# Kernel tuning notes

Hardware: AMD Instinct MI355X
Metric: run time of the kernel (lower is better)

## Reference

```python
import jax, jax.numpy as jnp
import numpy as np

# ---- constants (from init_kwargs / Config) ----
C = 10            # number of classes
P = 128           # fixed prototype capacity per class (masked)
GAMMA = 0.1
B_CONST = 10.0    # b
TAO = 1.0
BETA = 1.0
LAMBDA = 0.1
THRESHOLD = 40.0
EPS = 1e-6        # nn.PairwiseDistance eps (added to the difference)


def setup_inputs() -> dict:
    key = jax.random.key(0)
    k1, k2 = jax.random.split(key)
    features = jax.random.normal(k1, (8192, 512), dtype=jnp.float32)
    labels = jax.random.randint(k2, (8192,), 0, C, dtype=jnp.int32)
    return {"features": features, "labels": labels}


def _assign_prototypes(features, labels):
    """Sequential prototype assignment (faithful to assign_prototype).
    Fixed-capacity store: protos [C,P,D], counts [C,P], nproto [C]."""
    D = features.shape[1]
    protos = jnp.zeros((C, P, D), features.dtype)
    counts = jnp.zeros((C, P), jnp.int32)
    nproto = jnp.zeros((C,), jnp.int32)

    def step(carry, xs):
        protos, counts, nproto = carry
        f, l = xs
        row = protos[l]                       # [P, D]
        cnt = counts[l]                       # [P]
        n = nproto[l]
        valid = jnp.arange(P) < n
        d2 = jnp.sum((f[None, :] - row + EPS) ** 2, axis=-1)
        d2m = jnp.where(valid, d2, jnp.inf)
        idx = jnp.argmin(d2m)
        dmin = jnp.sqrt(d2m[idx])
        do_update = (n > 0) & (dmin < THRESHOLD)
        # running-mean update of closest prototype
        c = cnt[idx].astype(f.dtype)
        new_val = (row[idx] * c + f) / (c + 1.0)
        app_idx = jnp.minimum(n, P - 1)       # append slot (clamped; never hit with these settings)
        tgt_idx = jnp.where(do_update, idx, app_idx)
        tgt_val = jnp.where(do_update, new_val, f)
        tgt_cnt = jnp.where(do_update, cnt[idx] + 1, 1)
        row = row.at[tgt_idx].set(tgt_val)
        cnt = cnt.at[tgt_idx].set(tgt_cnt)
        n = jnp.where(do_update, n, jnp.minimum(n + 1, P))
        protos = protos.at[l].set(row)
        counts = counts.at[l].set(cnt)
        nproto = nproto.at[l].set(n)
        return (protos, counts, nproto), None

    (protos, counts, nproto), _ = jax.lax.scan(step, (protos, counts, nproto), (features, labels))
    return protos, nproto


def _forward(features, labels):
    # assign_prototype uses tensor(features).detach() -> stop_gradient
    protos, nproto = _assign_prototypes(jax.lax.stop_gradient(features), labels)
    B, D = features.shape
    flat = protos.reshape(C * P, D)
    valid = (jnp.arange(P)[None, :] < nproto[:, None]).reshape(C * P)

    # squared PairwiseDistance with eps added to the difference:
    # sum((f - p + eps)^2) = |f|^2 + |p|^2 - 2 f.p + 2*eps*(sum f - sum p) + D*eps^2
    f2 = jnp.sum(features ** 2, axis=-1)          # [B]
    p2 = jnp.sum(flat ** 2, axis=-1)              # [C*P]
    sf = jnp.sum(features, axis=-1)
    sp = jnp.sum(flat, axis=-1)
    d2 = (f2[:, None] + p2[None, :] - 2.0 * (features @ flat.T)
          + 2.0 * EPS * (sf[:, None] - sp[None, :]) + D * EPS * EPS)
    d2 = jnp.maximum(d2, 0.0)                     # [B, C*P]

    # dce loss: probability = 1e-6 + sum_label exp(-g d^2) / sum_all exp(-g d^2)
    expv = jnp.where(valid[None, :], jnp.exp(-GAMMA * d2), 0.0)
    per_class = expv.reshape(B, C, P).sum(-1)     # [B, C]
    one = per_class.sum(-1)                       # [B]
    num = jnp.take_along_axis(per_class, labels[:, None].astype(jnp.int32), axis=1)[:, 0]
    prob = 1e-6 + jnp.where(one > 0.0, num / one, one)
    dce_loss = jnp.sum(-jnp.log(prob))

    # pairwise loss: per sample, per existing class, min distance
    d2c = jnp.where(valid[None, :], d2, jnp.inf).reshape(B, C, P).min(-1)
    dmin = jnp.sqrt(d2c)                          # [B, C]
    sign = jnp.where(labels[:, None] == jnp.arange(C)[None, :], 1.0, -1.0)
    z = B_CONST - (TAO - dmin) * sign
    g = jnp.where(z > 10.0, z, jax.nn.softplus(BETA * z) / BETA)
    exists = nproto > 0                           # only classes present in all_prototypes
    pw_loss = jnp.sum(jnp.where(exists[None, :], g, 0.0))

    return dce_loss + LAMBDA * pw_loss


def reference(features, labels):
    return _forward(features, labels)
```

## Files before the change

kernel.cpp:

```cpp
#include <hip/hip_runtime.h>
#include <math.h>

#define NC 10
#define NP 128
#define ND 512
#define GAMMA  0.1f
#define BCONST 10.0f
#define TAO    1.0f
#define LAMBDA 0.1f
#define THR2   1600.0f
#define FEPS   1e-6f
#define NLDS   12
#define CH     16
#define MAXCH  512
#define IMAX   0x7FFFFFFF

__device__ __forceinline__ float allred64(float v) {
#pragma unroll
  for (int m = 1; m < 64; m <<= 1) v += __shfl_xor(v, m, 64);
  return v;
}

__global__ __launch_bounds__(256)
void ord_kernel(const int* __restrict__ labels, int B,
                int* __restrict__ order, int* __restrict__ cls_base,
                int* __restrict__ cls_cnt, int* __restrict__ fail_pos,
                int* __restrict__ nproto_g, float* __restrict__ out)
{
  __shared__ int lab[8192];
  __shared__ int wtot[4][NC];
  const int t = threadIdx.x, lane = t & 63, w = t >> 6;

  if (t < NC) { fail_pos[t] = IMAX; nproto_g[t] = 0; }
  if (t == 0) out[0] = 0.f;

  const int4* lp = (const int4*)labels;
  for (int i = t; i < (B >> 2); i += 256) {
    int4 v = lp[i];
    lab[i*4+0] = v.x; lab[i*4+1] = v.y; lab[i*4+2] = v.z; lab[i*4+3] = v.w;
  }
  for (int i = (B & ~3) + t; i < B; i += 256) lab[i] = labels[i];
  __syncthreads();

  const int segsz = (B + 255) >> 8;
  const int s0 = t * segsz, s1 = min(s0 + segsz, B);

  int loc[NC];
#pragma unroll
  for (int c = 0; c < NC; ++c) loc[c] = 0;
  for (int i = s0; i < s1; ++i) {
    int l = lab[i];
#pragma unroll
    for (int c = 0; c < NC; ++c) loc[c] += (l == c) ? 1 : 0;
  }

  int pre[NC];
#pragma unroll
  for (int c = 0; c < NC; ++c) pre[c] = loc[c];
#pragma unroll
  for (int m = 1; m < 64; m <<= 1) {
#pragma unroll
    for (int c = 0; c < NC; ++c) {
      int u = __shfl_up(pre[c], m, 64);
      if (lane >= m) pre[c] += u;
    }
  }
  if (lane == 63) {
#pragma unroll
    for (int c = 0; c < NC; ++c) wtot[w][c] = pre[c];
  }
  __syncthreads();

  int pos[NC];
  {
    int cb = 0;
#pragma unroll
    for (int c = 0; c < NC; ++c) {
      int tot = wtot[0][c] + wtot[1][c] + wtot[2][c] + wtot[3][c];
      int before = 0;
#pragma unroll
      for (int ww = 0; ww < 4; ++ww) before += (ww < w) ? wtot[ww][c] : 0;
      pos[c] = cb + before + (pre[c] - loc[c]);
      if (t == 0) { cls_base[c] = cb; cls_cnt[c] = tot; }
      cb += tot;
    }
  }

  for (int i = s0; i < s1; ++i) {
    int l = lab[i];
#pragma unroll
    for (int c = 0; c < NC; ++c)
      if (l == c) order[pos[c]++] = i;
  }
}

__global__ __launch_bounds__(64)
void chunksum_kernel(const float* __restrict__ feats, const int* __restrict__ order,
                     const int* __restrict__ cls_base, const int* __restrict__ cls_cnt,
                     float* __restrict__ chunksum)
{
  const int c = blockIdx.x / MAXCH, g = blockIdx.x % MAXCH;
  const int cnt = cls_cnt[c];
  const int nch = (cnt + CH - 1) / CH;
  if (g >= nch) return;
  const int base = cls_base[c], lane = threadIdx.x;
  const int k0 = g * CH, k1 = min(k0 + CH, cnt);
  int myidx = (lane < CH && k0 + lane < cnt) ? order[base + k0 + lane] : 0;

  float S[8] = {0, 0, 0, 0, 0, 0, 0, 0};
  int k = k0;
  for (; k + 4 <= k1; k += 4) {
    float4 A[4], Bv[4];
#pragma unroll
    for (int j = 0; j < 4; ++j) {
      int idx = __shfl(myidx, k + j - k0, 64);
      const float4* fp = (const float4*)(feats + (size_t)idx * ND + lane * 8);
      A[j] = fp[0]; Bv[j] = fp[1];
    }
#pragma unroll
    for (int j = 0; j < 4; ++j) {
      S[0]+=A[j].x; S[1]+=A[j].y; S[2]+=A[j].z; S[3]+=A[j].w;
      S[4]+=Bv[j].x; S[5]+=Bv[j].y; S[6]+=Bv[j].z; S[7]+=Bv[j].w;
    }
  }
  for (; k < k1; ++k) {
    int idx = __shfl(myidx, k - k0, 64);
    const float4* fp = (const float4*)(feats + (size_t)idx * ND + lane * 8);
    float4 a = fp[0], b = fp[1];
    S[0]+=a.x; S[1]+=a.y; S[2]+=a.z; S[3]+=a.w;
    S[4]+=b.x; S[5]+=b.y; S[6]+=b.z; S[7]+=b.w;
  }
  float4* cp = (float4*)(chunksum + ((size_t)c * MAXCH + g) * ND + lane * 8);
  cp[0] = make_float4(S[0], S[1], S[2], S[3]);
  cp[1] = make_float4(S[4], S[5], S[6], S[7]);
}

__global__ __launch_bounds__(64)
void verify_kernel(const float* __restrict__ feats, const int* __restrict__ order,
                   const int* __restrict__ cls_base, const int* __restrict__ cls_cnt,
                   const float* __restrict__ chunksum, int* __restrict__ fail_pos,
                   float* __restrict__ gproto, float* __restrict__ p2s,
                   float* __restrict__ sps, int* __restrict__ nproto_g)
{
  const int c = blockIdx.x / MAXCH, g = blockIdx.x % MAXCH;
  const int cnt = cls_cnt[c];
  const int nch = (cnt + CH - 1) / CH;
  if (g >= nch) return;
  const int base = cls_base[c], lane = threadIdx.x;
  const int k0 = g * CH, k1 = min(k0 + CH, cnt);
  int myidx = (lane < CH && k0 + lane < cnt) ? order[base + k0 + lane] : 0;

  float P[8] = {0, 0, 0, 0, 0, 0, 0, 0};
  {
    const float* cbase = chunksum + (size_t)c * MAXCH * ND + lane * 8;
    int j = 0;
    for (; j + 4 <= g; j += 4) {
      float4 A[4], Bv[4];
#pragma unroll
      for (int q = 0; q < 4; ++q) {
        const float4* pp = (const float4*)(cbase + (size_t)(j + q) * ND);
        A[q] = pp[0]; Bv[q] = pp[1];
      }
#pragma unroll
      for (int q = 0; q < 4; ++q) {
        P[0]+=A[q].x; P[1]+=A[q].y; P[2]+=A[q].z; P[3]+=A[q].w;
        P[4]+=Bv[q].x; P[5]+=Bv[q].y; P[6]+=Bv[q].z; P[7]+=Bv[q].w;
      }
    }
    for (; j < g; ++j) {
      const float4* pp = (const float4*)(cbase + (size_t)j * ND);
      float4 a = pp[0], b = pp[1];
      P[0]+=a.x; P[1]+=a.y; P[2]+=a.z; P[3]+=a.w;
      P[4]+=b.x; P[5]+=b.y; P[6]+=b.z; P[7]+=b.w;
    }
  }

  int k = k0;
  for (; k + 4 <= k1; k += 4) {
    float4 A[4], Bv[4];
#pragma unroll
    for (int j = 0; j < 4; ++j) {
      int idx = __shfl(myidx, k + j - k0, 64);
      const float4* fp = (const float4*)(feats + (size_t)idx * ND + lane * 8);
      A[j] = fp[0]; Bv[j] = fp[1];
    }
    float part[4];
#pragma unroll
    for (int j = 0; j < 4; ++j) {
      int kk = k + j;
      float f[8] = {A[j].x, A[j].y, A[j].z, A[j].w, Bv[j].x, Bv[j].y, Bv[j].z, Bv[j].w};
      if (kk > 0) {
        float inv = 1.f / (float)kk;
        float p = 0.f;
#pragma unroll
        for (int e = 0; e < 8; ++e) { float d = f[e] - P[e] * inv + FEPS; p += d * d; }
        part[j] = p;
      } else part[j] = 0.f;
#pragma unroll
      for (int e = 0; e < 8; ++e) P[e] += f[e];
    }
#pragma unroll
    for (int m = 1; m < 64; m <<= 1) {
#pragma unroll
      for (int j = 0; j < 4; ++j) part[j] += __shfl_xor(part[j], m, 64);
    }
    if (lane == 0) {
#pragma unroll
      for (int j = 0; j < 4; ++j) {
        int kk = k + j;
        if (kk > 0 && !(part[j] < THR2)) atomicMin(&fail_pos[c], kk);
      }
    }
  }
  for (; k < k1; ++k) {
    int idx = __shfl(myidx, k - k0, 64);
    const float4* fp = (const float4*)(feats + (size_t)idx * ND + lane * 8);
    float4 fa = fp[0], fb = fp[1];
    float f[8] = {fa.x, fa.y, fa.z, fa.w, fb.x, fb.y, fb.z, fb.w};
    if (k > 0) {
      float inv = 1.f / (float)k;
      float p = 0.f;
#pragma unroll
      for (int e = 0; e < 8; ++e) { float d = f[e] - P[e] * inv + FEPS; p += d * d; }
      float d2 = allred64(p);
      if (!(d2 < THR2) && lane == 0) atomicMin(&fail_pos[c], k);
    }
#pragma unroll
    for (int e = 0; e < 8; ++e) P[e] += f[e];
  }

  if (g == nch - 1) {
    float inv = 1.f / (float)cnt;
    float p[8];
#pragma unroll
    for (int e = 0; e < 8; ++e) p[e] = P[e] * inv;
    float4* gp = (float4*)(gproto + (size_t)c * NP * ND + lane * 8);
    gp[0] = make_float4(p[0], p[1], p[2], p[3]);
    gp[1] = make_float4(p[4], p[5], p[6], p[7]);
    float P2p = 0.f, SPp = 0.f;
#pragma unroll
    for (int e = 0; e < 8; ++e) { P2p += p[e]*p[e]; SPp += p[e]; }
    float P2 = allred64(P2p), SP = allred64(SPp);
    if (lane == 0) { p2s[c*NP] = P2; sps[c*NP] = SP; nproto_g[c] = 1; }
  }
}

__global__ __launch_bounds__(64)
void fallback_kernel(const float* __restrict__ feats, const int* __restrict__ order,
                     const int* __restrict__ cls_base, const int* __restrict__ cls_cnt,
                     const int* __restrict__ fail_pos,
                     float* __restrict__ gproto, float* __restrict__ p2s,
                     float* __restrict__ sps, int* __restrict__ nproto_g)
{
  const int c = blockIdx.x;
  if (fail_pos[c] == IMAX) return;

  __shared__ float ls_proto[NLDS][ND];
  __shared__ int   ls_cnt[NP];
  const int lane = threadIdx.x;
  const int base = cls_base[c], cnt = cls_cnt[c];

  float p0[8];
  int cnt0 = 0, n = 0;
  float fA[8], fB[8], fC[8];

  auto LOADF = [&](float (&buf)[8], int m) {
    int idx = order[base + m];
    const float4* fp = (const float4*)(feats + (size_t)idx * ND + lane * 8);
    float4 a = fp[0], b = fp[1];
    buf[0]=a.x; buf[1]=a.y; buf[2]=a.z; buf[3]=a.w;
    buf[4]=b.x; buf[5]=b.y; buf[6]=b.z; buf[7]=b.w;
  };

  auto STEP = [&](float (&f)[8]) {
    float best = 3.4e38f;
    int bidx = 0;
    if (n > 0) {
      float part = 0.f;
#pragma unroll
      for (int e = 0; e < 8; ++e) { float d = f[e] - p0[e] + FEPS; part += d * d; }
      best = allred64(part);
      for (int j = 1; j < n; ++j) {
        float pj[8];
        if (j <= NLDS) {
          const float4* pp = (const float4*)(&ls_proto[j-1][lane*8]);
          float4 a = pp[0], b = pp[1];
          pj[0]=a.x; pj[1]=a.y; pj[2]=a.z; pj[3]=a.w;
          pj[4]=b.x; pj[5]=b.y; pj[6]=b.z; pj[7]=b.w;
        } else {
          const float4* pp = (const float4*)(gproto + ((size_t)c*NP + j)*ND + lane*8);
          float4 a = pp[0], b = pp[1];
          pj[0]=a.x; pj[1]=a.y; pj[2]=a.z; pj[3]=a.w;
          pj[4]=b.x; pj[5]=b.y; pj[6]=b.z; pj[7]=b.w;
        }
        float part2 = 0.f;
#pragma unroll
        for (int e = 0; e < 8; ++e) { float d = f[e] - pj[e] + FEPS; part2 += d * d; }
        float tot = allred64(part2);
        if (tot < best) { best = tot; bidx = j; }
      }
    }
    if (n > 0 && best < THR2) {
      if (bidx == 0) {
        float cc = (float)cnt0, inv = 1.f / (cc + 1.f);
#pragma unroll
        for (int e = 0; e < 8; ++e) p0[e] = (p0[e]*cc + f[e]) * inv;
        cnt0++;
      } else {
        int ci = ls_cnt[bidx];
        float cc = (float)ci, inv = 1.f / (cc + 1.f);
        if (bidx <= NLDS) {
          float* row = &ls_proto[bidx-1][lane*8];
#pragma unroll
          for (int e = 0; e < 8; ++e) row[e] = (row[e]*cc + f[e]) * inv;
        } else {
          float* row = gproto + ((size_t)c*NP + bidx)*ND + lane*8;
#pragma unroll
          for (int e = 0; e < 8; ++e) row[e] = (row[e]*cc + f[e]) * inv;
        }
        if (lane == 0) ls_cnt[bidx] = ci + 1;
      }
    } else {
      int app = min(n, NP - 1);
      if (app == 0) {
#pragma unroll
        for (int e = 0; e < 8; ++e) p0[e] = f[e];
        cnt0 = 1;
      } else if (app <= NLDS) {
        float* row = &ls_proto[app-1][lane*8];
#pragma unroll
        for (int e = 0; e < 8; ++e) row[e] = f[e];
        if (lane == 0) ls_cnt[app] = 1;
      } else {
        float* row = gproto + ((size_t)c*NP + app)*ND + lane*8;
#pragma unroll
        for (int e = 0; e < 8; ++e) row[e] = f[e];
        if (lane == 0) ls_cnt[app] = 1;
      }
      n = min(n + 1, NP);
    }
  };

  if (cnt > 0) LOADF(fA, 0);
  if (cnt > 1) LOADF(fB, 1);
  if (cnt > 2) LOADF(fC, 2);
  int m = 0;
  while (m < cnt) {
    STEP(fA); ++m; if (m + 2 < cnt) LOADF(fA, m + 2);
    if (m >= cnt) break;
    STEP(fB); ++m; if (m + 2 < cnt) LOADF(fB, m + 2);
    if (m >= cnt) break;
    STEP(fC); ++m; if (m + 2 < cnt) LOADF(fC, m + 2);
  }

  for (int j = 0; j < n; ++j) {
    float pj[8];
    if (j == 0) {
#pragma unroll
      for (int e = 0; e < 8; ++e) pj[e] = p0[e];
    } else if (j <= NLDS) {
      const float4* pp = (const float4*)(&ls_proto[j-1][lane*8]);
      float4 a = pp[0], b = pp[1];
      pj[0]=a.x; pj[1]=a.y; pj[2]=a.z; pj[3]=a.w;
      pj[4]=b.x; pj[5]=b.y; pj[6]=b.z; pj[7]=b.w;
    } else {
      const float4* pp = (const float4*)(gproto + ((size_t)c*NP + j)*ND + lane*8);
      float4 a = pp[0], b = pp[1];
      pj[0]=a.x; pj[1]=a.y; pj[2]=a.z; pj[3]=a.w;
      pj[4]=b.x; pj[5]=b.y; pj[6]=b.z; pj[7]=b.w;
    }
    float4* gp = (float4*)(gproto + ((size_t)c*NP + j)*ND + lane*8);
    gp[0] = make_float4(pj[0], pj[1], pj[2], pj[3]);
    gp[1] = make_float4(pj[4], pj[5], pj[6], pj[7]);
    float P2p = 0.f, SPp = 0.f;
#pragma unroll
    for (int e = 0; e < 8; ++e) { P2p += pj[e]*pj[e]; SPp += pj[e]; }
    float P2 = allred64(P2p), SP = allred64(SPp);
    if (lane == 0) { p2s[c*NP + j] = P2; sps[c*NP + j] = SP; }
  }
  if (lane == 0) nproto_g[c] = n;
}

__global__ __launch_bounds__(256)
void loss_kernel(const float* __restrict__ feats, const int* __restrict__ labels, int B,
                 const float* __restrict__ gproto, const float* __restrict__ p2s,
                 const float* __restrict__ sps, const int* __restrict__ nproto_g,
                 float* __restrict__ out)
{
  __shared__ float bsum[4];
  const int lane = threadIdx.x & 63;
  const int wid  = threadIdx.x >> 6;
  const int gw   = blockIdx.x * 4 + wid;
  const int nw   = gridDim.x * 4;

  int np[NC];
  bool fast = true;
#pragma unroll
  for (int cc = 0; cc < NC; ++cc) { np[cc] = nproto_g[cc]; fast &= (np[cc] == 1); }

  float acc = 0.f;

  if (fast) {
    float p2v[NC], spv[NC];
#pragma unroll
    for (int cc = 0; cc < NC; ++cc) { p2v[cc] = p2s[cc*NP]; spv[cc] = sps[cc*NP]; }

    for (int b = gw; b < B; b += nw) {
      const float4* fp = (const float4*)(feats + (size_t)b * ND + lane * 8);
      float4 a4 = fp[0], b4 = fp[1];
      float f[8] = {a4.x, a4.y, a4.z, a4.w, b4.x, b4.y, b4.z, b4.w};
      int lab = labels[b];

      float v[12];
#pragma unroll
      for (int cc = 0; cc < NC; ++cc) {
        const float4* pp = (const float4*)(gproto + (size_t)cc * NP * ND + lane * 8);
        float4 pa = pp[0], pb = pp[1];
        v[cc] = f[0]*pa.x + f[1]*pa.y + f[2]*pa.z + f[3]*pa.w
              + f[4]*pb.x + f[5]*pb.y + f[6]*pb.z + f[7]*pb.w;
      }
      float f2p = 0.f, sfp = 0.f;
#pragma unroll
      for (int e = 0; e < 8; ++e) { f2p += f[e]*f[e]; sfp += f[e]; }
      v[10] = f2p; v[11] = sfp;

#pragma unroll
      for (int m = 1; m < 64; m <<= 1) {
#pragma unroll
        for (int q = 0; q < 12; ++q) v[q] += __shfl_xor(v[q], m, 64);
      }
      float f2 = v[10], sf = v[11];

      float one = 0.f, num = 0.f, pw = 0.f;
#pragma unroll
      for (int cc = 0; cc < NC; ++cc) {
        float d2 = f2 + p2v[cc] - 2.f*v[cc]
                 + 2.f*FEPS*(sf - spv[cc]) + (float)ND*FEPS*FEPS;
        d2 = fmaxf(d2, 0.f);
        float e = expf(-GAMMA * d2);
        one += e;
        if (cc == lab) num = e;
        float dmin = sqrtf(d2);
        float sign = (cc == lab) ? 1.f : -1.f;
        float z = BCONST - (TAO - dmin) * sign;
        float gg = (z > 10.f) ? z : log1pf(expf(z));
        pw += gg;
      }
      float prob = 1e-6f + ((one > 0.f) ? num / one : one);
      acc += -logf(prob) + LAMBDA * pw;
    }
  } else {
    for (int b = gw; b < B; b += nw) {
      const float4* fp = (const float4*)(feats + (size_t)b * ND + lane * 8);
      float4 a4 = fp[0], b4 = fp[1];
      float f[8] = {a4.x, a4.y, a4.z, a4.w, b4.x, b4.y, b4.z, b4.w};
      float f2p = 0.f, sfp = 0.f;
#pragma unroll
      for (int e = 0; e < 8; ++e) { f2p += f[e]*f[e]; sfp += f[e]; }
      float f2 = allred64(f2p);
      float sf = allred64(sfp);
      int lab = labels[b];

      float one = 0.f, num = 0.f, pw = 0.f;
      for (int cc = 0; cc < NC; ++cc) {
        int nn = np[cc];
        if (nn <= 0) continue;
        float sume = 0.f, bestd2 = 3.4e38f;
        for (int j = 0; j < nn; ++j) {
          const float4* pp = (const float4*)(gproto + ((size_t)cc*NP + j)*ND + lane*8);
          float4 pa = pp[0], pb = pp[1];
          float dp = f[0]*pa.x + f[1]*pa.y + f[2]*pa.z + f[3]*pa.w
                   + f[4]*pb.x + f[5]*pb.y + f[6]*pb.z + f[7]*pb.w;
          float dot = allred64(dp);
          float d2 = f2 + p2s[cc*NP + j] - 2.f*dot
                   + 2.f*FEPS*(sf - sps[cc*NP + j]) + (float)ND*FEPS*FEPS;
          d2 = fmaxf(d2, 0.f);
          sume  += expf(-GAMMA * d2);
          bestd2 = fminf(bestd2, d2);
        }
        one += sume;
        if (cc == lab) num = sume;
        float dmin = sqrtf(bestd2);
        float sign = (cc == lab) ? 1.f : -1.f;
        float z = BCONST - (TAO - dmin) * sign;
        float g = (z > 10.f) ? z : log1pf(expf(z));
        pw += g;
      }
      float prob = 1e-6f + ((one > 0.f) ? num / one : one);
      acc += -logf(prob) + LAMBDA * pw;
    }
  }

  if (lane == 0) bsum[wid] = acc;
  __syncthreads();
  if (threadIdx.x == 0) atomicAdd(out, bsum[0] + bsum[1] + bsum[2] + bsum[3]);
}

extern "C" void kernel_launch(void* const* d_in, const int* in_sizes, int n_in,
                              void* d_out, int out_size, void* d_ws, size_t ws_size,
                              hipStream_t stream) {
  const float* feats  = (const float*)d_in[0];
  const int*   labels = (const int*)d_in[1];
  int B = in_sizes[0] / ND;

  float* gproto   = (float*)d_ws;
  float* p2s      = gproto + (size_t)NC * NP * ND;
  float* sps      = p2s + NC * NP;
  float* chunksum = sps + NC * NP;
  int*   nproto_g = (int*)(chunksum + (size_t)NC * MAXCH * ND);
  int*   order    = nproto_g + NC;
  int*   cls_base = order + B;
  int*   cls_cnt  = cls_base + NC;
  int*   fail_pos = cls_cnt + NC;

  hipLaunchKernelGGL(ord_kernel, dim3(1), dim3(256), 0, stream,
                     labels, B, order, cls_base, cls_cnt, fail_pos,
                     nproto_g, (float*)d_out);
  hipLaunchKernelGGL(chunksum_kernel, dim3(NC * MAXCH), dim3(64), 0, stream,
                     feats, order, cls_base, cls_cnt, chunksum);
  hipLaunchKernelGGL(verify_kernel, dim3(NC * MAXCH), dim3(64), 0, stream,
                     feats, order, cls_base, cls_cnt, chunksum, fail_pos,
                     gproto, p2s, sps, nproto_g);
  hipLaunchKernelGGL(fallback_kernel, dim3(NC), dim3(64), 0, stream,
                     feats, order, cls_base, cls_cnt, fail_pos,
                     gproto, p2s, sps, nproto_g);
  hipLaunchKernelGGL(loss_kernel, dim3(2048), dim3(256), 0, stream,
                     feats, labels, B, gproto, p2s, sps, nproto_g, (float*)d_out);
}
```

Measured before the change: 88.82 us.

## Merge ordering, chunk-sum and fallback kernels into two compact-grid kernels

Drops the separate single-block label-ordering kernel and the fallback kernel. Each block of the chunk-sum and verify kernels now recomputes the per-class compaction into shared memory. Work is mapped onto a dense grid of 131 blocks with 4 waves each, instead of 5120 single-wave blocks where most exit early. The fallback now runs in the last-finishing wave of each failing class, found with a done counter, which cuts kernel launches and wasted block scheduling. The cost is that every block redundantly scans all the labels, and the fallback path leans on atomics and fences between waves of different blocks.

Measured after the change: 106.7 us. 20.1% more time.

```diff
diff --git a/kernel.cpp b/kernel.cpp
--- a/kernel.cpp
+++ b/kernel.cpp
@@ -12,100 +12,88 @@
 #define FEPS   1e-6f
 #define NLDS   12
 #define CH     16
-#define MAXCH  512
+#define WPB    4
+#define NBLK   131
 #define IMAX   0x7FFFFFFF
 
-__device__ __forceinline__ float allred64(float v) {
+__device__ __forceinline__ float allredf(float v) {
 #pragma unroll
   for (int m = 1; m < 64; m <<= 1) v += __shfl_xor(v, m, 64);
   return v;
 }
 
+#define COMPACT_BODY                                                          \
+  const int t = threadIdx.x, lane = t & 63, w = t >> 6;                       \
+  {                                                                           \
+    const int segsz = (B + 255) >> 8;                                         \
+    const int i0 = t * segsz, i1 = min(i0 + segsz, B);                        \
+    int loc[NC];                                                              \
+    _Pragma("unroll") for (int c = 0; c < NC; ++c) loc[c] = 0;                \
+    for (int i = i0; i < i1; ++i) {                                           \
+      int l = labels[i];                                                      \
+      _Pragma("unroll") for (int c = 0; c < NC; ++c) loc[c] += (l == c);      \
+    }                                                                         \
+    int pre[NC];                                                              \
+    _Pragma("unroll") for (int c = 0; c < NC; ++c) pre[c] = loc[c];           \
+    _Pragma("unroll") for (int m = 1; m < 64; m <<= 1) {                      \
+      _Pragma("unroll") for (int c = 0; c < NC; ++c) {                        \
+        int u = __shfl_up(pre[c], m, 64);                                     \
+        if (lane >= m) pre[c] += u;                                           \
+      }                                                                       \
+    }                                                                         \
+    if (lane == 63) {                                                         \
+      _Pragma("unroll") for (int c = 0; c < NC; ++c) wtot[w][c] = pre[c];     \
+    }                                                                         \
+    __syncthreads();                                                          \
+    int pos[NC];                                                              \
+    {                                                                         \
+      int cb = 0, crun = 0;                                                   \
+      _Pragma("unroll") for (int c = 0; c < NC; ++c) {                        \
+        int tot = wtot[0][c] + wtot[1][c] + wtot[2][c] + wtot[3][c];          \
+        int before = 0;                                                       \
+        _Pragma("unroll") for (int ww = 0; ww < 4; ++ww)                      \
+          before += (ww < w) ? wtot[ww][c] : 0;                               \
+        pos[c] = cb + before + (pre[c] - loc[c]);                             \
+        if (t == 0) { cb_s[c] = cb; cc_s[c] = tot; chb_s[c] = crun; }         \
+        cb += tot;                                                            \
+        crun += (tot + CH - 1) / CH;                                          \
+      }                                                                       \
+      if (t == 0) nchtot_s = crun;                                            \
+    }                                                                         \
+    for (int i = i0; i < i1; ++i) {                                           \
+      int l = labels[i];                                                      \
+      _Pragma("unroll") for (int c = 0; c < NC; ++c)                          \
+        if (l == c) list[pos[c]++] = i;                                       \
+    }                                                                         \
+  }                                                                           \
+  __syncthreads();
+
 __global__ __launch_bounds__(256)
-void ord_kernel(const int* __restrict__ labels, int B,
-                int* __restrict__ order, int* __restrict__ cls_base,
-                int* __restrict__ cls_cnt, int* __restrict__ fail_pos,
-                int* __restrict__ nproto_g, float* __restrict__ out)
+void sumc_kernel(const float* __restrict__ feats, const int* __restrict__ labels, int B,
+                 float* __restrict__ chunksum, int* __restrict__ done_g,
+                 int* __restrict__ fail_g, int* __restrict__ nproto_g,
+                 float* __restrict__ out)
 {
-  __shared__ int lab[8192];
+  __shared__ int list[8192];
   __shared__ int wtot[4][NC];
-  const int t = threadIdx.x, lane = t & 63, w = t >> 6;
-
-  if (t < NC) { fail_pos[t] = IMAX; nproto_g[t] = 0; }
-  if (t == 0) out[0] = 0.f;
-
-  const int4* lp = (const int4*)labels;
-  for (int i = t; i < (B >> 2); i += 256) {
-    int4 v = lp[i];
-    lab[i*4+0] = v.x; lab[i*4+1] = v.y; lab[i*4+2] = v.z; lab[i*4+3] = v.w;
-  }
-  for (int i = (B & ~3) + t; i < B; i += 256) lab[i] = labels[i];
-  __syncthreads();
-
-  const int segsz = (B + 255) >> 8;
-  const int s0 = t * segsz, s1 = min(s0 + segsz, B);
-
-  int loc[NC];
-#pragma unroll
-  for (int c = 0; c < NC; ++c) loc[c] = 0;
-  for (int i = s0; i < s1; ++i) {
-    int l = lab[i];
-#pragma unroll
-    for (int c = 0; c < NC; ++c) loc[c] += (l == c) ? 1 : 0;
-  }
-
-  int pre[NC];
-#pragma unroll
-  for (int c = 0; c < NC; ++c) pre[c] = loc[c];
-#pragma unroll
-  for (int m = 1; m < 64; m <<= 1) {
-#pragma unroll
-    for (int c = 0; c < NC; ++c) {
-      int u = __shfl_up(pre[c], m, 64);
-      if (lane >= m) pre[c] += u;
-    }
-  }
-  if (lane == 63) {
-#pragma unroll
-    for (int c = 0; c < NC; ++c) wtot[w][c] = pre[c];
-  }
-  __syncthreads();
-
-  int pos[NC];
-  {
-    int cb = 0;
-#pragma unroll
-    for (int c = 0; c < NC; ++c) {
-      int tot = wtot[0][c] + wtot[1][c] + wtot[2][c] + wtot[3][c];
-      int before = 0;
-#pragma unroll
-      for (int ww = 0; ww < 4; ++ww) before += (ww < w) ? wtot[ww][c] : 0;
-      pos[c] = cb + before + (pre[c] - loc[c]);
-      if (t == 0) { cls_base[c] = cb; cls_cnt[c] = tot; }
-      cb += tot;
-    }
-  }
-
-  for (int i = s0; i < s1; ++i) {
-    int l = lab[i];
-#pragma unroll
-    for (int c = 0; c < NC; ++c)
-      if (l == c) order[pos[c]++] = i;
-  }
-}
-
-__global__ __launch_bounds__(64)
-void chunksum_kernel(const float* __restrict__ feats, const int* __restrict__ order,
-                     const int* __restrict__ cls_base, const int* __restrict__ cls_cnt,
-                     float* __restrict__ chunksum)
-{
-  const int c = blockIdx.x / MAXCH, g = blockIdx.x % MAXCH;
-  const int cnt = cls_cnt[c];
-  const int nch = (cnt + CH - 1) / CH;
-  if (g >= nch) return;
-  const int base = cls_base[c], lane = threadIdx.x;
+  __shared__ int cb_s[NC], cc_s[NC], chb_s[NC];
+  __shared__ int nchtot_s;
+
+  COMPACT_BODY
+
+  if (blockIdx.x == 0 && t == 0) {
+    out[0] = 0.f;
+    for (int i = 0; i < NC; ++i) { done_g[i] = 0; fail_g[i] = 0; nproto_g[i] = 0; }
+  }
+
+  const int gwid = blockIdx.x * WPB + w;
+  if (gwid >= nchtot_s) return;
+
+  int c = 0;
+  while (c + 1 < NC && chb_s[c + 1] <= gwid) ++c;
+  const int g = gwid - chb_s[c];
+  const int cnt = cc_s[c], base = cb_s[c];
   const int k0 = g * CH, k1 = min(k0 + CH, cnt);
-  int myidx = (lane < CH && k0 + lane < cnt) ? order[base + k0 + lane] : 0;
 
   float S[8] = {0, 0, 0, 0, 0, 0, 0, 0};
   int k = k0;
@@ -113,7 +101,7 @@
     float4 A[4], Bv[4];
 #pragma unroll
     for (int j = 0; j < 4; ++j) {
-      int idx = __shfl(myidx, k + j - k0, 64);
+      int idx = list[base + k + j];
       const float4* fp = (const float4*)(feats + (size_t)idx * ND + lane * 8);
       A[j] = fp[0]; Bv[j] = fp[1];
     }
@@ -124,35 +112,48 @@
     }
   }
   for (; k < k1; ++k) {
-    int idx = __shfl(myidx, k - k0, 64);
+    int idx = list[base + k];
     const float4* fp = (const float4*)(feats + (size_t)idx * ND + lane * 8);
     float4 a = fp[0], b = fp[1];
     S[0]+=a.x; S[1]+=a.y; S[2]+=a.z; S[3]+=a.w;
     S[4]+=b.x; S[5]+=b.y; S[6]+=b.z; S[7]+=b.w;
   }
-  float4* cp = (float4*)(chunksum + ((size_t)c * MAXCH + g) * ND + lane * 8);
+  float4* cp = (float4*)(chunksum + (size_t)gwid * ND + lane * 8);
   cp[0] = make_float4(S[0], S[1], S[2], S[3]);
   cp[1] = make_float4(S[4], S[5], S[6], S[7]);
 }
 
-__global__ __launch_bounds__(64)
-void verify_kernel(const float* __restrict__ feats, const int* __restrict__ order,
-                   const int* __restrict__ cls_base, const int* __restrict__ cls_cnt,
-                   const float* __restrict__ chunksum, int* __restrict__ fail_pos,
-                   float* __restrict__ gproto, float* __restrict__ p2s,
-                   float* __restrict__ sps, int* __restrict__ nproto_g)
+__global__ __launch_bounds__(256)
+void verify_kernel(const float* __restrict__ feats, const int* __restrict__ labels, int B,
+                   const float* __restrict__ chunksum, int* __restrict__ done_g,
+                   int* __restrict__ fail_g, float* __restrict__ gproto,
+                   float* __restrict__ p2s, float* __restrict__ sps,
+                   int* __restrict__ nproto_g)
 {
-  const int c = blockIdx.x / MAXCH, g = blockIdx.x % MAXCH;
-  const int cnt = cls_cnt[c];
-  const int nch = (cnt + CH - 1) / CH;
-  if (g >= nch) return;
-  const int base = cls_base[c], lane = threadIdx.x;
+  __shared__ int   list[8192];
+  __shared__ int   wtot[4][NC];
+  __shared__ int   cb_s[NC], cc_s[NC], chb_s[NC];
+  __shared__ int   nchtot_s;
+  __shared__ float ls_proto[NLDS][ND];
+  __shared__ int   ls_cnt[NP];
+  __shared__ int   fblock;
+
+  if (threadIdx.x == 0) fblock = 0;
+  COMPACT_BODY
+
+  const int gwid = blockIdx.x * WPB + w;
+  if (gwid >= nchtot_s) return;
+
+  int c = 0;
+  while (c + 1 < NC && chb_s[c + 1] <= gwid) ++c;
+  const int g = gwid - chb_s[c];
+  const int cnt = cc_s[c], base = cb_s[c];
+  const int nchc = (cnt + CH - 1) / CH;
   const int k0 = g * CH, k1 = min(k0 + CH, cnt);
-  int myidx = (lane < CH && k0 + lane < cnt) ? order[base + k0 + lane] : 0;
 
   float P[8] = {0, 0, 0, 0, 0, 0, 0, 0};
   {
-    const float* cbase = chunksum + (size_t)c * MAXCH * ND + lane * 8;
+    const float* cbase = chunksum + (size_t)chb_s[c] * ND + lane * 8;
     int j = 0;
     for (; j + 4 <= g; j += 4) {
       float4 A[4], Bv[4];
@@ -180,7 +181,7 @@
     float4 A[4], Bv[4];
 #pragma unroll
     for (int j = 0; j < 4; ++j) {
-      int idx = __shfl(myidx, k + j - k0, 64);
+      int idx = list[base + k + j];
       const float4* fp = (const float4*)(feats + (size_t)idx * ND + lane * 8);
       A[j] = fp[0]; Bv[j] = fp[1];
     }
@@ -190,10 +191,10 @@
       int kk = k + j;
       float f[8] = {A[j].x, A[j].y, A[j].z, A[j].w, Bv[j].x, Bv[j].y, Bv[j].z, Bv[j].w};
       if (kk > 0) {
-        float inv = 1.f / (float)kk;
+        float invk = 1.f / (float)kk;
         float p = 0.f;
 #pragma unroll
-        for (int e = 0; e < 8; ++e) { float d = f[e] - P[e] * inv + FEPS; p += d * d; }
+        for (int e = 0; e < 8; ++e) { float d = f[e] - P[e] * invk + FEPS; p += d * d; }
         part[j] = p;
       } else part[j] = 0.f;
 #pragma unroll
@@ -208,177 +209,178 @@
 #pragma unroll
       for (int j = 0; j < 4; ++j) {
         int kk = k + j;
-        if (kk > 0 && !(part[j] < THR2)) atomicMin(&fail_pos[c], kk);
+        if (kk > 0 && !(part[j] < THR2)) atomicOr(&fail_g[c], 1);
       }
     }
   }
   for (; k < k1; ++k) {
-    int idx = __shfl(myidx, k - k0, 64);
+    int idx = list[base + k];
     const float4* fp = (const float4*)(feats + (size_t)idx * ND + lane * 8);
     float4 fa = fp[0], fb = fp[1];
     float f[8] = {fa.x, fa.y, fa.z, fa.w, fb.x, fb.y, fb.z, fb.w};
     if (k > 0) {
-      float inv = 1.f / (float)k;
+      float invk = 1.f / (float)k;
       float p = 0.f;
 #pragma unroll
-      for (int e = 0; e < 8; ++e) { float d = f[e] - P[e] * inv + FEPS; p += d * d; }
-      float d2 = allred64(p);
-      if (!(d2 < THR2) && lane == 0) atomicMin(&fail_pos[c], k);
+      for (int e = 0; e < 8; ++e) { float d = f[e] - P[e] * invk + FEPS; p += d * d; }
+      float d2 = allredf(p);
+      if (!(d2 < THR2) && lane == 0) atomicOr(&fail_g[c], 1);
     }
 #pragma unroll
     for (int e = 0; e < 8; ++e) P[e] += f[e];
   }
 
-  if (g == nch - 1) {
-    float inv = 1.f / (float)cnt;
+  if (g == nchc - 1) {
+    float invc = 1.f / (float)cnt;
     float p[8];
 #pragma unroll
-    for (int e = 0; e < 8; ++e) p[e] = P[e] * inv;
+    for (int e = 0; e < 8; ++e) p[e] = P[e] * invc;
     float4* gp = (float4*)(gproto + (size_t)c * NP * ND + lane * 8);
     gp[0] = make_float4(p[0], p[1], p[2], p[3]);
     gp[1] = make_float4(p[4], p[5], p[6], p[7]);
     float P2p = 0.f, SPp = 0.f;
 #pragma unroll
     for (int e = 0; e < 8; ++e) { P2p += p[e]*p[e]; SPp += p[e]; }
-    float P2 = allred64(P2p), SP = allred64(SPp);
+    float P2 = allredf(P2p), SP = allredf(SPp);
     if (lane == 0) { p2s[c*NP] = P2; sps[c*NP] = SP; nproto_g[c] = 1; }
   }
-}
-
-__global__ __launch_bounds__(64)
-void fallback_kernel(const float* __restrict__ feats, const int* __restrict__ order,
-                     const int* __restrict__ cls_base, const int* __restrict__ cls_cnt,
-                     const int* __restrict__ fail_pos,
-                     float* __restrict__ gproto, float* __restrict__ p2s,
-                     float* __restrict__ sps, int* __restrict__ nproto_g)
-{
-  const int c = blockIdx.x;
-  if (fail_pos[c] == IMAX) return;
-
-  __shared__ float ls_proto[NLDS][ND];
-  __shared__ int   ls_cnt[NP];
-  const int lane = threadIdx.x;
-  const int base = cls_base[c], cnt = cls_cnt[c];
-
-  float p0[8];
-  int cnt0 = 0, n = 0;
-  float fA[8], fB[8], fC[8];
-
-  auto LOADF = [&](float (&buf)[8], int m) {
-    int idx = order[base + m];
-    const float4* fp = (const float4*)(feats + (size_t)idx * ND + lane * 8);
-    float4 a = fp[0], b = fp[1];
-    buf[0]=a.x; buf[1]=a.y; buf[2]=a.z; buf[3]=a.w;
-    buf[4]=b.x; buf[5]=b.y; buf[6]=b.z; buf[7]=b.w;
-  };
-
-  auto STEP = [&](float (&f)[8]) {
-    float best = 3.4e38f;
-    int bidx = 0;
-    if (n > 0) {
-      float part = 0.f;
-#pragma unroll
-      for (int e = 0; e < 8; ++e) { float d = f[e] - p0[e] + FEPS; part += d * d; }
-      best = allred64(part);
-      for (int j = 1; j < n; ++j) {
-        float pj[8];
-        if (j <= NLDS) {
-          const float4* pp = (const float4*)(&ls_proto[j-1][lane*8]);
-          float4 a = pp[0], b = pp[1];
-          pj[0]=a.x; pj[1]=a.y; pj[2]=a.z; pj[3]=a.w;
-          pj[4]=b.x; pj[5]=b.y; pj[6]=b.z; pj[7]=b.w;
+
+  __threadfence();
+  int old = 0;
+  if (lane == 0) old = atomicAdd(&done_g[c], 1);
+  old = __shfl(old, 0, 64);
+  if (old != nchc - 1) return;
+  __threadfence();
+  int fv = 0;
+  if (lane == 0) fv = atomicOr(&fail_g[c], 0);
+  fv = __shfl(fv, 0, 64);
+  if (!fv) return;
+
+  if (lane == 0) { while (atomicCAS(&fblock, 0, 1) != 0) {} }
+
+  {
+    float p0[8];
+    int cnt0 = 0, n = 0;
+    float fA[8], fB[8], fC[8];
+
+    auto LOADF = [&](float (&buf)[8], int m) {
+      int idx = list[base + m];
+      const float4* fp = (const float4*)(feats + (size_t)idx * ND + lane * 8);
+      float4 a = fp[0], b = fp[1];
+      buf[0]=a.x; buf[1]=a.y; buf[2]=a.z; buf[3]=a.w;
+      buf[4]=b.x; buf[5]=b.y; buf[6]=b.z; buf[7]=b.w;
+    };
+    auto STEP = [&](float (&f)[8]) {
+      float best = 3.4e38f;
+      int bidx = 0;
+      if (n > 0) {
+        float part = 0.f;
+#pragma unroll
+        for (int e = 0; e < 8; ++e) { float d = f[e] - p0[e] + FEPS; part += d * d; }
+        best = allredf(part);
+        for (int j = 1; j < n; ++j) {
+          float pj[8];
+          if (j <= NLDS) {
+            const float4* pp = (const float4*)(&ls_proto[j-1][lane*8]);
+            float4 a = pp[0], b = pp[1];
+            pj[0]=a.x; pj[1]=a.y; pj[2]=a.z; pj[3]=a.w;
+            pj[4]=b.x; pj[5]=b.y; pj[6]=b.z; pj[7]=b.w;
+          } else {
+            const float4* pp = (const float4*)(gproto + ((size_t)c*NP + j)*ND + lane*8);
+            float4 a = pp[0], b = pp[1];
+            pj[0]=a.x; pj[1]=a.y; pj[2]=a.z; pj[3]=a.w;
+            pj[4]=b.x; pj[5]=b.y; pj[6]=b.z; pj[7]=b.w;
+          }
+          float part2 = 0.f;
+#pragma unroll
+          for (int e = 0; e < 8; ++e) { float d = f[e] - pj[e] + FEPS; part2 += d * d; }
+          float tot = allredf(part2);
+          if (tot < best) { best = tot; bidx = j; }
+        }
+      }
+      if (n > 0 && best < THR2) {
+        if (bidx == 0) {
+          float cc = (float)cnt0, iv = 1.f / (cc + 1.f);
+#pragma unroll
+          for (int e = 0; e < 8; ++e) p0[e] = (p0[e]*cc + f[e]) * iv;
+          cnt0++;
         } else {
-          const float4* pp = (const float4*)(gproto + ((size_t)c*NP + j)*ND + lane*8);
-          float4 a = pp[0], b = pp[1];
-          pj[0]=a.x; pj[1]=a.y; pj[2]=a.z; pj[3]=a.w;
-          pj[4]=b.x; pj[5]=b.y; pj[6]=b.z; pj[7]=b.w;
+          int ci = ls_cnt[bidx];
+          float cc = (float)ci, iv = 1.f / (cc + 1.f);
+          if (bidx <= NLDS) {
+            float* row = &ls_proto[bidx-1][lane*8];
+#pragma unroll
+            for (int e = 0; e < 8; ++e) row[e] = (row[e]*cc + f[e]) * iv;
+          } else {
+            float* row = gproto + ((size_t)c*NP + bidx)*ND + lane*8;
+#pragma unroll
+            for (int e = 0; e < 8; ++e) row[e] = (row[e]*cc + f[e]) * iv;
+          }
+          if (lane == 0) ls_cnt[bidx] = ci + 1;
         }
-        float part2 = 0.f;
-#pragma unroll
-        for (int e = 0; e < 8; ++e) { float d = f[e] - pj[e] + FEPS; part2 += d * d; }
-        float tot = allred64(part2);
-        if (tot < best) { best = tot; bidx = j; }
-      }
-    }
-    if (n > 0 && best < THR2) {
-      if (bidx == 0) {
-        float cc = (float)cnt0, inv = 1.f / (cc + 1.f);
-#pragma unroll
-        for (int e = 0; e < 8; ++e) p0[e] = (p0[e]*cc + f[e]) * inv;
-        cnt0++;
       } else {
-        int ci = ls_cnt[bidx];
-        float cc = (float)ci, inv = 1.f / (cc + 1.f);
-        if (bidx <= NLDS) {
-          float* row = &ls_proto[bidx-1][lane*8];
-#pragma unroll
-          for (int e = 0; e < 8; ++e) row[e] = (row[e]*cc + f[e]) * inv;
+        int app = min(n, NP - 1);
+        if (app == 0) {
+#pragma unroll
+          for (int e = 0; e < 8; ++e) p0[e] = f[e];
+          cnt0 = 1;
+        } else if (app <= NLDS) {
+          float* row = &ls_proto[app-1][lane*8];
+#pragma unroll
+          for (int e = 0; e < 8; ++e) row[e] = f[e];
+          if (lane == 0) ls_cnt[app] = 1;
         } else {
-          float* row = gproto + ((size_t)c*NP + bidx)*ND + lane*8;
-#pragma unroll
-          for (int e = 0; e < 8; ++e) row[e] = (row[e]*cc + f[e]) * inv;
+          float* row = gproto + ((size_t)c*NP + app)*ND + lane*8;
+#pragma unroll
+          for (int e = 0; e < 8; ++e) row[e] = f[e];
+          if (lane == 0) ls_cnt[app] = 1;
         }
-        if (lane == 0) ls_cnt[bidx] = ci + 1;
-      }
-    } else {
-      int app = min(n, NP - 1);
-      if (app == 0) {
-#pragma unroll
-        for (int e = 0; e < 8; ++e) p0[e] = f[e];
-        cnt0 = 1;
-      } else if (app <= NLDS) {
-        float* row = &ls_proto[app-1][lane*8];
-#pragma unroll
-        for (int e = 0; e < 8; ++e) row[e] = f[e];
-        if (lane == 0) ls_cnt[app] = 1;
+        n = min(n + 1, NP);
+      }
+    };
+
+    if (cnt > 0) LOADF(fA, 0);
+    if (cnt > 1) LOADF(fB, 1);
+    if (cnt > 2) LOADF(fC, 2);
+    int m = 0;
+    while (m < cnt) {
+      STEP(fA); ++m; if (m + 2 < cnt) LOADF(fA, m + 2);
+      if (m >= cnt) break;
+      STEP(fB); ++m; if (m + 2 < cnt) LOADF(fB, m + 2);
+      if (m >= cnt) break;
+      STEP(fC); ++m; if (m + 2 < cnt) LOADF(fC, m + 2);
+    }
+
+    for (int j = 0; j < n; ++j) {
+      float pj[8];
+      if (j == 0) {
+#pragma unroll
+        for (int e = 0; e < 8; ++e) pj[e] = p0[e];
+      } else if (j <= NLDS) {
+        const float4* pp = (const float4*)(&ls_proto[j-1][lane*8]);
+        float4 a = pp[0], b = pp[1];
+        pj[0]=a.x; pj[1]=a.y; pj[2]=a.z; pj[3]=a.w;
+        pj[4]=b.x; pj[5]=b.y; pj[6]=b.z; pj[7]=b.w;
       } else {
-        float* row = gproto + ((size_t)c*NP + app)*ND + lane*8;
-#pragma unroll
-        for (int e = 0; e < 8; ++e) row[e] = f[e];
-        if (lane == 0) ls_cnt[app] = 1;
-      }
-      n = min(n + 1, NP);
-    }
-  };
-
-  if (cnt > 0) LOADF(fA, 0);
-  if (cnt > 1) LOADF(fB, 1);
-  if (cnt > 2) LOADF(fC, 2);
-  int m = 0;
-  while (m < cnt) {
-    STEP(fA); ++m; if (m + 2 < cnt) LOADF(fA, m + 2);
-    if (m >= cnt) break;
-    STEP(fB); ++m; if (m + 2 < cnt) LOADF(fB, m + 2);
-    if (m >= cnt) break;
-    STEP(fC); ++m; if (m + 2 < cnt) LOADF(fC, m + 2);
-  }
-
-  for (int j = 0; j < n; ++j) {
-    float pj[8];
-    if (j == 0) {
-#pragma unroll
-      for (int e = 0; e < 8; ++e) pj[e] = p0[e];
-    } else if (j <= NLDS) {
-      const float4* pp = (const float4*)(&ls_proto[j-1][lane*8]);
-      float4 a = pp[0], b = pp[1];
-      pj[0]=a.x; pj[1]=a.y; pj[2]=a.z; pj[3]=a.w;
-      pj[4]=b.x; pj[5]=b.y; pj[6]=b.z; pj[7]=b.w;
-    } else {
-      const float4* pp = (const float4*)(gproto + ((size_t)c*NP + j)*ND + lane*8);
-      float4 a = pp[0], b = pp[1];
-      pj[0]=a.x; pj[1]=a.y; pj[2]=a.z; pj[3]=a.w;
-      pj[4]=b.x; pj[5]=b.y; pj[6]=b.z; pj[7]=b.w;
-    }
-    float4* gp = (float4*)(gproto + ((size_t)c*NP + j)*ND + lane*8);
-    gp[0] = make_float4(pj[0], pj[1], pj[2], pj[3]);
-    gp[1] = make_float4(pj[4], pj[5], pj[6], pj[7]);
-    float P2p = 0.f, SPp = 0.f;
-#pragma unroll
-    for (int e = 0; e < 8; ++e) { P2p += pj[e]*pj[e]; SPp += pj[e]; }
-    float P2 = allred64(P2p), SP = allred64(SPp);
-    if (lane == 0) { p2s[c*NP + j] = P2; sps[c*NP + j] = SP; }
-  }
-  if (lane == 0) nproto_g[c] = n;
+        const float4* pp = (const float4*)(gproto + ((size_t)c*NP + j)*ND + lane*8);
+        float4 a = pp[0], b = pp[1];
+        pj[0]=a.x; pj[1]=a.y; pj[2]=a.z; pj[3]=a.w;
+        pj[4]=b.x; pj[5]=b.y; pj[6]=b.z; pj[7]=b.w;
+      }
+      float4* gp = (float4*)(gproto + ((size_t)c*NP + j)*ND + lane*8);
+      gp[0] = make_float4(pj[0], pj[1], pj[2], pj[3]);
+      gp[1] = make_float4(pj[4], pj[5], pj[6], pj[7]);
+      float P2p = 0.f, SPp = 0.f;
+#pragma unroll
+      for (int e = 0; e < 8; ++e) { P2p += pj[e]*pj[e]; SPp += pj[e]; }
+      float P2 = allredf(P2p), SP = allredf(SPp);
+      if (lane == 0) { p2s[c*NP + j] = P2; sps[c*NP + j] = SP; }
+    }
+    if (lane == 0) nproto_g[c] = n;
+  }
+
+  __threadfence_block();
+  if (lane == 0) atomicExch(&fblock, 0);
 }
 
 __global__ __launch_bounds__(256)
@@ -399,18 +401,15 @@
   for (int cc = 0; cc < NC; ++cc) { np[cc] = nproto_g[cc]; fast &= (np[cc] == 1); }
 
   float acc = 0.f;
-
   if (fast) {
     float p2v[NC], spv[NC];
 #pragma unroll
     for (int cc = 0; cc < NC; ++cc) { p2v[cc] = p2s[cc*NP]; spv[cc] = sps[cc*NP]; }
-
     for (int b = gw; b < B; b += nw) {
       const float4* fp = (const float4*)(feats + (size_t)b * ND + lane * 8);
       float4 a4 = fp[0], b4 = fp[1];
       float f[8] = {a4.x, a4.y, a4.z, a4.w, b4.x, b4.y, b4.z, b4.w};
       int lab = labels[b];
-
       float v[12];
 #pragma unroll
       for (int cc = 0; cc < NC; ++cc) {
@@ -423,14 +422,12 @@
 #pragma unroll
       for (int e = 0; e < 8; ++e) { f2p += f[e]*f[e]; sfp += f[e]; }
       v[10] = f2p; v[11] = sfp;
-
 #pragma unroll
       for (int m = 1; m < 64; m <<= 1) {
 #pragma unroll
         for (int q = 0; q < 12; ++q) v[q] += __shfl_xor(v[q], m, 64);
       }
       float f2 = v[10], sf = v[11];
-
       float one = 0.f, num = 0.f, pw = 0.f;
 #pragma unroll
       for (int cc = 0; cc < NC; ++cc) {
@@ -457,10 +454,9 @@
       float f2p = 0.f, sfp = 0.f;
 #pragma unroll
       for (int e = 0; e < 8; ++e) { f2p += f[e]*f[e]; sfp += f[e]; }
-      float f2 = allred64(f2p);
-      float sf = allred64(sfp);
+      float f2 = allredf(f2p);
+      float sf = allredf(sfp);
       int lab = labels[b];
-
       float one = 0.f, num = 0.f, pw = 0.f;
       for (int cc = 0; cc < NC; ++cc) {
         int nn = np[cc];
@@ -471,7 +467,7 @@
           float4 pa = pp[0], pb = pp[1];
           float dp = f[0]*pa.x + f[1]*pa.y + f[2]*pa.z + f[3]*pa.w
                    + f[4]*pb.x + f[5]*pb.y + f[6]*pb.z + f[7]*pb.w;
-          float dot = allred64(dp);
+          float dot = allredf(dp);
           float d2 = f2 + p2s[cc*NP + j] - 2.f*dot
                    + 2.f*FEPS*(sf - sps[cc*NP + j]) + (float)ND*FEPS*FEPS;
           d2 = fmaxf(d2, 0.f);
@@ -502,28 +498,22 @@
   const float* feats  = (const float*)d_in[0];
   const int*   labels = (const int*)d_in[1];
   int B = in_sizes[0] / ND;
+  const int maxwin = (B + CH - 1) / CH + NC;
 
   float* gproto   = (float*)d_ws;
   float* p2s      = gproto + (size_t)NC * NP * ND;
   float* sps      = p2s + NC * NP;
   float* chunksum = sps + NC * NP;
-  int*   nproto_g = (int*)(chunksum + (size_t)NC * MAXCH * ND);
-  int*   order    = nproto_g + NC;
-  int*   cls_base = order + B;
-  int*   cls_cnt  = cls_base + NC;
-  int*   fail_pos = cls_cnt + NC;
-
-  hipLaunchKernelGGL(ord_kernel, dim3(1), dim3(256), 0, stream,
-                     labels, B, order, cls_base, cls_cnt, fail_pos,
-                     nproto_g, (float*)d_out);
-  hipLaunchKernelGGL(chunksum_kernel, dim3(NC * MAXCH), dim3(64), 0, stream,
-                     feats, order, cls_base, cls_cnt, chunksum);
-  hipLaunchKernelGGL(verify_kernel, dim3(NC * MAXCH), dim3(64), 0, stream,
-                     feats, order, cls_base, cls_cnt, chunksum, fail_pos,
-                     gproto, p2s, sps, nproto_g);
-  hipLaunchKernelGGL(fallback_kernel, dim3(NC), dim3(64), 0, stream,
-                     feats, order, cls_base, cls_cnt, fail_pos,
+  int*   done_g   = (int*)(chunksum + (size_t)maxwin * ND);
+  int*   fail_g   = done_g + NC;
+  int*   nproto_g = fail_g + NC;
+  float* outf     = (float*)d_out;
+
+  hipLaunchKernelGGL(sumc_kernel, dim3(NBLK), dim3(256), 0, stream,
+                     feats, labels, B, chunksum, done_g, fail_g, nproto_g, outf);
+  hipLaunchKernelGGL(verify_kernel, dim3(NBLK), dim3(256), 0, stream,
+                     feats, labels, B, chunksum, done_g, fail_g,
                      gproto, p2s, sps, nproto_g);
   hipLaunchKernelGGL(loss_kernel, dim3(2048), dim3(256), 0, stream,
-                     feats, labels, B, gproto, p2s, sps, nproto_g, (float*)d_out);
+                     feats, labels, B, gproto, p2s, sps, nproto_g, outf);
 }
```
